# Kernel tuning notes

Hardware: AMD Instinct MI355X
Metric: run time of the kernel (lower is better)

Reference implementation:

```python
import jax, jax.numpy as jnp
import numpy as np

B, T, N, FIN, FOUT, EDGE_DIM = 8, 16, 256, 32, 32, 16


def setup_inputs() -> dict:
    key = jax.random.key(0)
    ks = jax.random.split(key, 8)
    def xavier(k, shape):
        fan_in, fan_out = shape[0], shape[1]
        limit = float(np.sqrt(6.0 / (fan_in + fan_out)))
        return jax.random.uniform(k, shape, jnp.float32, -limit, limit)
    return {
        "x": jax.random.normal(ks[0], (B, T, N, FIN), jnp.float32),
        "adj": jax.random.uniform(ks[1], (N, N), jnp.float32),
        # edge_net: Linear(1, edge_dim) -> GELU -> Linear(edge_dim, Fin*Fout)
        "w1": xavier(ks[2], (1, EDGE_DIM)),
        "b1": jnp.zeros((EDGE_DIM,), jnp.float32),
        "w2": xavier(ks[3], (EDGE_DIM, FIN * FOUT)),
        "b2": jnp.zeros((FIN * FOUT,), jnp.float32),
        # node_lin: Linear(Fin, Fout)
        "node_w": xavier(ks[4], (FIN, FOUT)),
        "node_b": jnp.zeros((FOUT,), jnp.float32),
    }


def reference(x, adj, w1, b1, w2, b2, node_w, node_b):
    # edge-conditioned weights: (N, N, Fin, Fout)
    h = jax.nn.gelu(adj[:, :, None] * w1[0] + b1, approximate=False)  # (N,N,E)
    edge_w = (h @ w2 + b2).reshape(N, N, FIN, FOUT)
    # msg[b,t,i,j,:] = sum_f x[b,t,j,f] * edge_w[i,j,f,:]; agg = sum_j msg
    agg = jnp.einsum("btjf,ijfo->btio", x, edge_w)  # (B,T,N,Fout)
    y = jax.nn.gelu(x @ node_w + node_b + agg, approximate=False)
    return y
```

## Files before the change

### kernel.cpp

```cpp
#include <hip/hip_runtime.h>
#include <math.h>

#define NB    256
#define FINN  32
#define FOUTN 32
#define BT    128


typedef __attribute__((ext_vector_type(8))) short short8;
typedef __attribute__((ext_vector_type(4))) float floatx4;

#define MFMA16(a,b,c) __builtin_amdgcn_mfma_f32_16x16x32_bf16((a),(b),(c),0,0,0)

#define BARRIER() asm volatile("s_waitcnt lgkmcnt(0)\n\ts_barrier" ::: "memory")

__device__ __forceinline__ float gelu_f(float v) {
    return 0.5f * v * (1.0f + erff(v * 0.70710678118654752f));
}
__device__ __forceinline__ ushort f2bf(float x) {
    union { float f; unsigned u; } v; v.f = x;
    unsigned r = (v.u + 0x7FFFu + ((v.u >> 16) & 1u)) >> 16;
    return (ushort)r;
}
__device__ __forceinline__ uint2 pack4(floatx4 d) {
    uint2 p;
    p.x = (unsigned)f2bf(d[0]) | ((unsigned)f2bf(d[1]) << 16);
    p.y = (unsigned)f2bf(d[2]) | ((unsigned)f2bf(d[3]) << 16);
    return p;
}

__global__ __launch_bounds__(256) void prep_kernel(
        const float* __restrict__ x,   const float* __restrict__ adj,
        const float* __restrict__ w1,  const float* __restrict__ b1,
        const float* __restrict__ w2,  const float* __restrict__ b2,
        const float* __restrict__ node_w, const float* __restrict__ node_b,
        ushort* __restrict__ Hf, ushort* __restrict__ w2f,
        ushort* __restrict__ xaf, ushort* __restrict__ nwf,
        float* __restrict__ bias2g) {
    int bid = blockIdx.x;
    int tid = threadIdx.x;

    if (bid < 128) {
        __shared__ float adjs[16][264];
        __shared__ float w1s[16], b1s[16];
        int it = bid & 15;
        int kq8 = bid >> 4;
        if (tid < 16) { w1s[tid] = w1[tid]; b1s[tid] = b1[tid]; }
        #pragma unroll
        for (int q = 0; q < 4; ++q) {
            int u = q * 256 + tid;
            int row = u >> 6, c4 = u & 63;
            *(float4*)&adjs[row][c4 * 4] =
                ((const float4*)(adj + ((size_t)it * 16 + row) * 256))[c4];
        }
        __syncthreads();
        #pragma unroll
        for (int q = 0; q < 4; ++q) {
            int u = q * 256 + tid;
            int ks = kq8 * 16 + (u >> 6);
            int lane = u & 63;
            int m = lane & 15, quad = lane >> 4;
            int e = ks >> 3;
            int j0 = (ks & 7) * 32 + quad * 8;
            float w = w1s[e], b = b1s[e];
            ushort tmp[8];
            #pragma unroll
            for (int d = 0; d < 8; ++d)
                tmp[d] = f2bf(gelu_f(adjs[m][j0 + d] * w + b));
            *(int4*)(Hf + (((size_t)it * 128 + ks) * 64 + lane) * 8) = *(int4*)tmp;
        }
        return;
    }
    if (bid < 160) {
        int wv = tid >> 6, lane = tid & 63, m = lane & 15, quad = lane >> 4;
        int bt = (bid - 128) * 4 + wv;
        #pragma unroll
        for (int jt = 0; jt < 16; ++jt) {
            const float* xs = x + ((size_t)bt * NB + jt * 16 + m) * FINN + quad * 8;
            float4 lo = *(const float4*)xs;
            float4 hi = *(const float4*)(xs + 4);
            ushort tmp[8];
            tmp[0]=f2bf(lo.x); tmp[1]=f2bf(lo.y); tmp[2]=f2bf(lo.z); tmp[3]=f2bf(lo.w);
            tmp[4]=f2bf(hi.x); tmp[5]=f2bf(hi.y); tmp[6]=f2bf(hi.z); tmp[7]=f2bf(hi.w);
            *(int4*)(xaf + (((size_t)bt * 16 + jt) * 64 + lane) * 8) = *(int4*)tmp;
        }
        return;
    }
    if (bid < 288) {
        __shared__ float Sp[8][32];
        __shared__ float Svs[32];
        int bt = bid - 160;
        int f = tid & 31, grp = tid >> 5;
        float s = 0.f;
        for (int j = grp; j < NB; j += 8)
            s += x[((size_t)bt * NB + j) * FINN + f];
        Sp[grp][f] = s;
        __syncthreads();
        if (tid < 32) {
            float s2 = 0.f;
            #pragma unroll
            for (int g = 0; g < 8; ++g) s2 += Sp[g][tid];
            Svs[tid] = s2;
        }
        __syncthreads();
        if (tid < 32) {
            float bb = node_b[tid];
            #pragma unroll
            for (int f2 = 0; f2 < FINN; ++f2)
                bb += Svs[f2] * b2[f2 * FOUTN + tid];
            bias2g[bt * 32 + tid] = bb;
        }
        return;
    }
    for (int s = 0; s < 2048; s += 256) {
        int slot = s + tid;
        int e = slot >> 7, r = slot & 127;
        int ot = r >> 6, lane = r & 63;
        int m = lane & 15, quad = lane >> 4;
        const float* src = w2 + (size_t)e * 1024 + (quad * 8) * 32 + ot * 16 + m;
        ushort tmp[8];
        #pragma unroll
        for (int i = 0; i < 8; ++i) tmp[i] = f2bf(src[i * 32]);
        *(int4*)(w2f + (size_t)slot * 8) = *(int4*)tmp;
    }
    if (tid < 128) {
        int ot = tid >> 6, lane = tid & 63, m = lane & 15, q = lane >> 4;
        ushort tmp[8];
        #pragma unroll
        for (int d = 0; d < 8; ++d)
            tmp[d] = f2bf(node_w[(q * 8 + d) * 32 + ot * 16 + m]);
        *(int4*)(nwf + tid * 8) = *(int4*)tmp;
    }
}

__global__ __launch_bounds__(512, 4) void main_kernel(
        const ushort* __restrict__ Hf,  const ushort* __restrict__ w2f,
        const ushort* __restrict__ xaf, float* __restrict__ Cp) {
    __shared__ ushort Bsl[2][8][2][512];

    int bt   = blockIdx.x;
    int kq   = blockIdx.y;
    int tid  = threadIdx.x;
    int wv   = tid >> 6;
    int lane = tid & 63;
    int m    = lane & 15;
    int quad = lane >> 4;

    short8 xfr[2];
    #pragma unroll
    for (int t = 0; t < 2; ++t)
        xfr[t] = *(const short8*)(xaf + (((size_t)bt * 16 + wv + 8 * t) * 64 + lane) * 8);
    const int qc = (wv & 1) * 2 + (quad >> 1);
    const int dp = (quad & 1) * 4;
    const int jp0 = (wv >> 1);

    const ushort* Ha = Hf + ((size_t)(2 * wv + 0) * 128) * 512 + (size_t)lane * 8;
    const ushort* Hb = Hf + ((size_t)(2 * wv + 1) * 128) * 512 + (size_t)lane * 8;
    const ushort* Wl = w2f + (size_t)lane * 8;

    short8 areg[4][2];
    floatx4 acc[2][2] = {};

    #define ALOADS(slot, s_)                                                  \
    {                                                                         \
        int ks_ = kq * 32 + (s_); if (ks_ > 127) ks_ = 127;                   \
        areg[slot][0] = *(const short8*)(Ha + (size_t)ks_ * 512);             \
        areg[slot][1] = *(const short8*)(Hb + (size_t)ks_ * 512);             \
    }
    #define PRODUCE(bp, wf0, wf1)                                             \
    {                                                                         \
        _Pragma("unroll")                                                     \
        for (int t = 0; t < 2; ++t) {                                         \
            int jp = jp0 + 4 * t;                                             \
            floatx4 z = {0.f, 0.f, 0.f, 0.f};                                 \
            floatx4 d0 = MFMA16(xfr[t], wf0, z);                              \
            floatx4 d1 = MFMA16(xfr[t], wf1, z);                              \
            *(uint2*)((bp) + jp * 1024 +       (qc * 16 + m) * 8 + dp) = pack4(d0); \
            *(uint2*)((bp) + jp * 1024 + 512 + (qc * 16 + m) * 8 + dp) = pack4(d1); \
        }                                                                     \
    }

    ALOADS(0, 0);
    ALOADS(1, 1);
    {
        short8 wf0 = *(const short8*)(Wl + (size_t)(kq * 4) * 1024);
        short8 wf1 = *(const short8*)(Wl + (size_t)(kq * 4) * 1024 + 512);
        PRODUCE((ushort*)Bsl, wf0, wf1);
    }
    BARRIER();

    #pragma unroll 1
    for (int w = 0; w < 4; ++w) {
        int en = kq * 4 + ((w < 3) ? (w + 1) : 3);
        short8 wf0 = *(const short8*)(Wl + (size_t)en * 1024);
        short8 wf1 = *(const short8*)(Wl + (size_t)en * 1024 + 512);

        ushort* Bb = (ushort*)Bsl + (w & 1) * 8192;
        #pragma unroll
        for (int kk = 0; kk < 8; ++kk) {
            ALOADS((kk + 2) & 3, w * 8 + kk + 2);
            short8 b0 = *(const short8*)(Bb + kk * 1024 + lane * 8);
            short8 b1 = *(const short8*)(Bb + kk * 1024 + 512 + lane * 8);
            acc[0][0] = MFMA16(areg[kk & 3][0], b0, acc[0][0]);
            acc[0][1] = MFMA16(areg[kk & 3][0], b1, acc[0][1]);
            acc[1][0] = MFMA16(areg[kk & 3][1], b0, acc[1][0]);
            acc[1][1] = MFMA16(areg[kk & 3][1], b1, acc[1][1]);
        }
        if (w < 3) {
            ushort* Bn = (ushort*)Bsl + ((w + 1) & 1) * 8192;
            PRODUCE(Bn, wf0, wf1);
        }
        BARRIER();
    }

    #pragma unroll
    for (int t = 0; t < 2; ++t)
        #pragma unroll
        for (int oh = 0; oh < 2; ++oh)
            #pragma unroll
            for (int r = 0; r < 4; ++r) {
                int i = (2 * wv + t) * 16 + quad * 4 + r;
                Cp[(((size_t)bt * NB + i) * 4 + kq) * FOUTN + oh * 16 + m]
                    = acc[t][oh][r];
            }
    #undef ALOADS
    #undef PRODUCE
}

__global__ __launch_bounds__(256) void epi_kernel(
        const ushort* __restrict__ xaf, const ushort* __restrict__ nwf,
        const float* __restrict__ bias2g, const float* __restrict__ Cp,
        float* __restrict__ out) {
    int bt   = blockIdx.x;
    int ih   = blockIdx.y;
    int tid  = threadIdx.x;
    int wv   = tid >> 6;
    int lane = tid & 63;
    int m    = lane & 15;
    int quad = lane >> 4;

    short8 nb0 = *(const short8*)(nwf + (size_t)lane * 8);
    short8 nb1 = *(const short8*)(nwf + ((size_t)64 + lane) * 8);

    #pragma unroll
    for (int t = 0; t < 2; ++t) {
        int it = ih * 8 + wv * 2 + t;
        short8 xa = *(const short8*)(xaf + (((size_t)bt * 16 + it) * 64 + lane) * 8);
        #pragma unroll
        for (int tn = 0; tn < 2; ++tn) {
            floatx4 z = {0.f, 0.f, 0.f, 0.f};
            floatx4 ea = MFMA16(xa, tn ? nb1 : nb0, z);
            float bz = bias2g[bt * 32 + tn * 16 + m];
            #pragma unroll
            for (int r = 0; r < 4; ++r) {
                int i = it * 16 + quad * 4 + r;
                float s = ea[r] + bz;
                #pragma unroll
                for (int kqi = 0; kqi < 4; ++kqi)
                    s += Cp[(((size_t)bt * NB + i) * 4 + kqi) * FOUTN + tn * 16 + m];
                out[((size_t)bt * NB + i) * FOUTN + tn * 16 + m] = gelu_f(s);
            }
        }
    }
}

extern "C" void kernel_launch(void* const* d_in, const int* in_sizes, int n_in,
                              void* d_out, int out_size, void* d_ws, size_t ws_size,
                              hipStream_t stream) {
    const float* x      = (const float*)d_in[0];
    const float* adj    = (const float*)d_in[1];
    const float* w1     = (const float*)d_in[2];
    const float* b1     = (const float*)d_in[3];
    const float* w2     = (const float*)d_in[4];
    const float* b2     = (const float*)d_in[5];
    const float* node_w = (const float*)d_in[6];
    const float* node_b = (const float*)d_in[7];
    float* out = (float*)d_out;

    ushort* Hf     = (ushort*)d_ws;
    ushort* w2f    = Hf + (size_t)16 * 128 * 512;
    ushort* xaf    = w2f + 16384;
    ushort* nwf    = xaf + (size_t)128 * 16 * 512;
    float*  bias2g = (float*)(nwf + 1024);
    float*  Cp     = bias2g + 128 * 32;

    hipLaunchKernelGGL(prep_kernel, dim3(289), dim3(256), 0, stream,
                       x, adj, w1, b1, w2, b2, node_w, node_b,
                       Hf, w2f, xaf, nwf, bias2g);
    hipLaunchKernelGGL(main_kernel, dim3(BT, 4), dim3(512), 0, stream,
                       Hf, w2f, xaf, Cp);
    hipLaunchKernelGGL(epi_kernel, dim3(BT, 2), dim3(256), 0, stream,
                       xaf, nwf, bias2g, Cp, out);
}
```

Measured before the change: 104.6 us.

## Double main kernel block to 1024 threads, one row tile per wave

The main kernel now launches 16 waves per block instead of 8, so each wave owns a single 16-row tile of H and a single x fragment instead of two. The A-operand prefetch is deepened from a 4-slot ring to 8 registers preloaded ahead of the loop. Per-wave work and register pressure drop and more waves are available to hide latency. The cost is a larger block per workgroup and a __launch_bounds__(1024,4) request that may not be satisfiable, which could force register spills or limit residency.

```diff
diff --git a/kernel.cpp b/kernel.cpp
--- a/kernel.cpp
+++ b/kernel.cpp
@@ -133,7 +133,7 @@
     }
 }
 
-__global__ __launch_bounds__(512, 4) void main_kernel(
+__global__ __launch_bounds__(1024, 4) void main_kernel(
         const ushort* __restrict__ Hf,  const ushort* __restrict__ w2f,
         const ushort* __restrict__ xaf, float* __restrict__ Cp) {
     __shared__ ushort Bsl[2][8][2][512];
@@ -146,42 +146,33 @@
     int m    = lane & 15;
     int quad = lane >> 4;
 
-    short8 xfr[2];
-    #pragma unroll
-    for (int t = 0; t < 2; ++t)
-        xfr[t] = *(const short8*)(xaf + (((size_t)bt * 16 + wv + 8 * t) * 64 + lane) * 8);
-    const int qc = (wv & 1) * 2 + (quad >> 1);
-    const int dp = (quad & 1) * 4;
-    const int jp0 = (wv >> 1);
-
-    const ushort* Ha = Hf + ((size_t)(2 * wv + 0) * 128) * 512 + (size_t)lane * 8;
-    const ushort* Hb = Hf + ((size_t)(2 * wv + 1) * 128) * 512 + (size_t)lane * 8;
+    short8 xfr = *(const short8*)(xaf + (((size_t)bt * 16 + wv) * 64 + lane) * 8);
+    const int qc  = (wv & 1) * 2 + (quad >> 1);
+    const int dp  = (quad & 1) * 4;
+    const int jp0 = wv >> 1;
+
+    const ushort* Ha = Hf + (size_t)wv * 128 * 512 + (size_t)lane * 8;
     const ushort* Wl = w2f + (size_t)lane * 8;
 
-    short8 areg[4][2];
-    floatx4 acc[2][2] = {};
-
-    #define ALOADS(slot, s_)                                                  \
+    short8 areg[8];
+    floatx4 acc[2] = {};
+
+    #define ALOAD(slot, s_)                                                   \
     {                                                                         \
         int ks_ = kq * 32 + (s_); if (ks_ > 127) ks_ = 127;                   \
-        areg[slot][0] = *(const short8*)(Ha + (size_t)ks_ * 512);             \
-        areg[slot][1] = *(const short8*)(Hb + (size_t)ks_ * 512);             \
+        areg[slot] = *(const short8*)(Ha + (size_t)ks_ * 512);                \
     }
     #define PRODUCE(bp, wf0, wf1)                                             \
     {                                                                         \
-        _Pragma("unroll")                                                     \
-        for (int t = 0; t < 2; ++t) {                                         \
-            int jp = jp0 + 4 * t;                                             \
-            floatx4 z = {0.f, 0.f, 0.f, 0.f};                                 \
-            floatx4 d0 = MFMA16(xfr[t], wf0, z);                              \
-            floatx4 d1 = MFMA16(xfr[t], wf1, z);                              \
-            *(uint2*)((bp) + jp * 1024 +       (qc * 16 + m) * 8 + dp) = pack4(d0); \
-            *(uint2*)((bp) + jp * 1024 + 512 + (qc * 16 + m) * 8 + dp) = pack4(d1); \
-        }                                                                     \
-    }
-
-    ALOADS(0, 0);
-    ALOADS(1, 1);
+        floatx4 z = {0.f, 0.f, 0.f, 0.f};                                     \
+        floatx4 d0 = MFMA16(xfr, wf0, z);                                     \
+        floatx4 d1 = MFMA16(xfr, wf1, z);                                     \
+        *(uint2*)((bp) + jp0 * 1024 +       (qc * 16 + m) * 8 + dp) = pack4(d0); \
+        *(uint2*)((bp) + jp0 * 1024 + 512 + (qc * 16 + m) * 8 + dp) = pack4(d1); \
+    }
+
+    #pragma unroll
+    for (int s = 0; s < 8; ++s) ALOAD(s, s);
     {
         short8 wf0 = *(const short8*)(Wl + (size_t)(kq * 4) * 1024);
         short8 wf1 = *(const short8*)(Wl + (size_t)(kq * 4) * 1024 + 512);
@@ -198,13 +189,12 @@
         ushort* Bb = (ushort*)Bsl + (w & 1) * 8192;
         #pragma unroll
         for (int kk = 0; kk < 8; ++kk) {
-            ALOADS((kk + 2) & 3, w * 8 + kk + 2);
+            short8 a = areg[kk];
+            ALOAD(kk, w * 8 + kk + 8);
             short8 b0 = *(const short8*)(Bb + kk * 1024 + lane * 8);
             short8 b1 = *(const short8*)(Bb + kk * 1024 + 512 + lane * 8);
-            acc[0][0] = MFMA16(areg[kk & 3][0], b0, acc[0][0]);
-            acc[0][1] = MFMA16(areg[kk & 3][0], b1, acc[0][1]);
-            acc[1][0] = MFMA16(areg[kk & 3][1], b0, acc[1][0]);
-            acc[1][1] = MFMA16(areg[kk & 3][1], b1, acc[1][1]);
+            acc[0] = MFMA16(a, b0, acc[0]);
+            acc[1] = MFMA16(a, b1, acc[1]);
         }
         if (w < 3) {
             ushort* Bn = (ushort*)Bsl + ((w + 1) & 1) * 8192;
@@ -214,16 +204,14 @@
     }
 
     #pragma unroll
-    for (int t = 0; t < 2; ++t)
-        #pragma unroll
-        for (int oh = 0; oh < 2; ++oh)
-            #pragma unroll
-            for (int r = 0; r < 4; ++r) {
-                int i = (2 * wv + t) * 16 + quad * 4 + r;
-                Cp[(((size_t)bt * NB + i) * 4 + kq) * FOUTN + oh * 16 + m]
-                    = acc[t][oh][r];
-            }
-    #undef ALOADS
+    for (int oh = 0; oh < 2; ++oh)
+        #pragma unroll
+        for (int r = 0; r < 4; ++r) {
+            int i = wv * 16 + quad * 4 + r;
+            Cp[(((size_t)bt * NB + i) * 4 + kq) * FOUTN + oh * 16 + m]
+                = acc[oh][r];
+        }
+    #undef ALOAD
     #undef PRODUCE
 }
 
@@ -287,7 +275,7 @@
     hipLaunchKernelGGL(prep_kernel, dim3(289), dim3(256), 0, stream,
                        x, adj, w1, b1, w2, b2, node_w, node_b,
                        Hf, w2f, xaf, nwf, bias2g);
-    hipLaunchKernelGGL(main_kernel, dim3(BT, 4), dim3(512), 0, stream,
+    hipLaunchKernelGGL(main_kernel, dim3(BT, 4), dim3(1024), 0, stream,
                        Hf, w2f, xaf, Cp);
     hipLaunchKernelGGL(epi_kernel, dim3(BT, 2), dim3(256), 0, stream,
                        xaf, nwf, bias2g, Cp, out);
```

Result: no change. 106.1 us (+1.4%).
